# Kernel optimization log

Hardware: AMD Instinct MI355X
Metric: run time of the kernel (lower is better)

Reference implementation:

```python
import jax, jax.numpy as jnp
from jax import lax
import numpy as np

T, N, H, C = 1000, 64, 1024, 256

def setup_inputs() -> dict:
    key = jax.random.key(0)
    k0, k1, k2, k3, k4 = jax.random.split(key, 5)
    s = 0.05
    return {
        "encoder_output": jax.random.normal(k0, (T, N, H), dtype=jnp.float32),
        "W_ih": jax.random.normal(k1, (3 * C, H), dtype=jnp.float32) * s,  # [r|z|n] input weights
        "W_hh": jax.random.normal(k2, (3 * C, C), dtype=jnp.float32) * s,
        "b_ih": jax.random.normal(k3, (3 * C,), dtype=jnp.float32) * s,
        "b_hh": jax.random.normal(k4, (3 * C,), dtype=jnp.float32) * s,
    }

def reference(encoder_output, W_ih, W_hh, b_ih, b_hh):
    # Batched input projection over all timesteps: [T,N,3C]
    xp = jnp.einsum('tnh,gh->tng', encoder_output, W_ih) + b_ih
    c = W_hh.shape[1]

    def step(h, xp_t):
        gh = h @ W_hh.T + b_hh                      # [N,3C]
        xr, xz, xn = jnp.split(xp_t, 3, axis=-1)
        hr, hz, hn = jnp.split(gh, 3, axis=-1)
        r = jax.nn.sigmoid(xr + hr)
        z = jax.nn.sigmoid(xz + hz)
        n = jnp.tanh(xn + r * hn)
        h_new = (1.0 - z) * n + z * h
        return h_new, h_new

    h0 = jnp.zeros((encoder_output.shape[1], c), dtype=encoder_output.dtype)
    _, out = lax.scan(step, h0, xp)                 # out: [T,N,C]
    return jax.nn.log_softmax(out, axis=2)
```

## Files before the change

### kernel.cpp

```cpp
#include <hip/hip_runtime.h>
#include <stdint.h>

#define T_STEPS 1000
#define NB      64
#define HDIM    1024
#define CDIM    256
#define G3      768
#define LOG2E   1.44269504088896340736f

typedef float f32x4  __attribute__((ext_vector_type(4)));
typedef short bf16x8 __attribute__((ext_vector_type(8)));
typedef int   i32x4  __attribute__((ext_vector_type(4)));

__device__ __forceinline__ float bf2f(unsigned short u) {
    union { unsigned int i; float f; } v; v.i = ((unsigned int)u) << 16; return v.f;
}
__device__ __forceinline__ unsigned short f2bf(float f) {
    union { float f; unsigned int i; } v; v.f = f;
    unsigned int r = v.i + 0x7fffu + ((v.i >> 16) & 1u);
    return (unsigned short)(r >> 16);
}

__device__ __forceinline__ int pack4(i32x4 a) {
#if __has_builtin(__builtin_amdgcn_permlane16_swap) && __has_builtin(__builtin_amdgcn_permlane32_swap)
    auto y01 = __builtin_amdgcn_permlane16_swap(a[0], a[1], false, false);
    auto y23 = __builtin_amdgcn_permlane16_swap(a[2], a[3], false, false);
    auto p   = __builtin_amdgcn_permlane32_swap(y01[0], y23[0], false, false);
    return p[0];
#else
    const int lane = threadIdx.x & 63;
    const int l15  = lane & 15;
    const int r1b = __shfl(a[1], l15, 64);
    const int r3b = __shfl(a[3], l15, 64);
    const int x01 = (lane < 16) ? a[0] : r1b;
    const int x23 = (lane < 16) ? a[2] : r3b;
    const int lo  = __shfl(x23, lane & 31, 64);
    return (lane < 32) ? x01 : lo;
#endif
}

__global__ __launch_bounds__(256) void cvt_wih(
    const float* __restrict__ wih, unsigned short* __restrict__ wih_bf)
{
    int idx = blockIdx.x * 256 + threadIdx.x;
    wih_bf[idx] = f2bf(wih[idx]);
}

__global__ __launch_bounds__(64) void quant_whh(
    const float* __restrict__ whh, signed char* __restrict__ wq,
    float* __restrict__ dscale)
{
    const int g    = blockIdx.x;
    const int lane = threadIdx.x;
    const float4 w = *(const float4*)(whh + (size_t)g * CDIM + lane * 4);
    float m = fmaxf(fmaxf(fabsf(w.x), fabsf(w.y)), fmaxf(fabsf(w.z), fabsf(w.w)));
    #pragma unroll
    for (int s = 32; s > 0; s >>= 1) m = fmaxf(m, __shfl_xor(m, s, 64));
    const float inv = (m > 0.f) ? 127.f / m : 0.f;
    char4 q;
    q.x = (signed char)(int)rintf(w.x * inv);
    q.y = (signed char)(int)rintf(w.y * inv);
    q.z = (signed char)(int)rintf(w.z * inv);
    q.w = (signed char)(int)rintf(w.w * inv);
    *(char4*)(wq + (size_t)g * CDIM + lane * 4) = q;
    if (lane == 0) dscale[g] = m / (127.f * 127.f);
}

__global__ __launch_bounds__(256) void xproj_gemm(
    const float* __restrict__ enc,
    const unsigned short* __restrict__ wih,
    const float* __restrict__ bih,
    unsigned short* __restrict__ xp2)
{
    const int gt_base = blockIdx.x * 64;
    const int t       = blockIdx.y;
    const int tid  = threadIdx.x;
    const int w    = tid >> 6;
    const int lane = tid & 63;
    const int q    = lane >> 4, l15 = lane & 15;

    __shared__ unsigned short As[64][72];
    __shared__ unsigned short Bs[64][72];

    const f32x4 zero4 = {0.f, 0.f, 0.f, 0.f};
    f32x4 acc[4] = {zero4, zero4, zero4, zero4};

    const int arow = tid >> 4;
    const int acol = (tid & 15) * 4;
    const int brow = tid >> 3;
    const int bcol = (tid & 7) * 8;

    for (int kt = 0; kt < 16; ++kt) {
        const int k0 = kt * 64;
        __syncthreads();
        #pragma unroll
        for (int i = 0; i < 4; ++i) {
            const int r = arow + i * 16;
            const float4 av = *(const float4*)(enc + (size_t)(t * 64 + r) * HDIM + k0 + acol);
            ushort4 u;
            u.x = f2bf(av.x); u.y = f2bf(av.y); u.z = f2bf(av.z); u.w = f2bf(av.w);
            *(ushort4*)(&As[r][acol]) = u;
        }
        #pragma unroll
        for (int i = 0; i < 2; ++i) {
            const int r = brow + i * 32;
            const uint4 bv = *(const uint4*)(wih + (size_t)(gt_base + r) * HDIM + k0 + bcol);
            *(uint4*)(&Bs[r][bcol]) = bv;
        }
        __syncthreads();
        #pragma unroll
        for (int kk = 0; kk < 2; ++kk) {
            const bf16x8 a = *(const bf16x8*)(&As[16 * w + l15][kk * 32 + q * 8]);
            #pragma unroll
            for (int g = 0; g < 4; ++g) {
                const bf16x8 b = *(const bf16x8*)(&Bs[16 * g + l15][kk * 32 + q * 8]);
                acc[g] = __builtin_amdgcn_mfma_f32_16x16x32_bf16(a, b, acc[g], 0, 0, 0);
            }
        }
    }

    #pragma unroll
    for (int g = 0; g < 4; ++g) {
        const int gg = gt_base + 16 * g + l15;
        const float bias = bih[gg];
        ushort4 u;
        u.x = f2bf(acc[g][0] + bias);
        u.y = f2bf(acc[g][1] + bias);
        u.z = f2bf(acc[g][2] + bias);
        u.w = f2bf(acc[g][3] + bias);
        *(ushort4*)(xp2 + ((size_t)((t * 16 + 4 * w + q) * G3 + gg)) * 4) = u;
    }
}

__global__ void __launch_bounds__(1024)
__attribute__((amdgpu_waves_per_eu(4, 4)))
gru_scan(
    const unsigned short* __restrict__ xp2,
    const signed char* __restrict__ wq,
    const float* __restrict__ dscale,
    const float* __restrict__ bhh,
    float* __restrict__ out)
{
    const int wg   = blockIdx.x;
    const int tid  = threadIdx.x;
    const int wv   = tid >> 6;
    const int lane = tid & 63;
    const int q    = lane >> 4, l15 = lane & 15;
    const int jc   = 16 * wv + l15;

    __shared__ __align__(16) signed char hbuf[2][16][304];

    i32x4 W[3][4];
    float d[3], bh[3];
    #pragma unroll
    for (int s = 0; s < 3; ++s) {
        const int g = 256 * s + jc;
        d[s]  = dscale[g];
        bh[s] = bhh[g];
        #pragma unroll
        for (int kk = 0; kk < 4; ++kk)
            W[s][kk] = *(const i32x4*)(wq + (size_t)g * CDIM + kk * 64 + q * 16);
    }
    #pragma unroll
    for (int s = 0; s < 3; ++s)
        asm volatile("" : "+v"(W[s][0]), "+v"(W[s][1]),
                          "+v"(W[s][2]), "+v"(W[s][3]));

    float h = 0.f;

    for (int i = tid; i < 2 * 16 * 304; i += 1024) ((signed char*)hbuf)[i] = 0;
    __syncthreads();

    unsigned short xc[3];
    {
        const unsigned short* xpt = xp2 + (size_t)wg * (G3 * 4);
        #pragma unroll
        for (int s = 0; s < 3; ++s)
            xc[s] = xpt[(256 * s + jc) * 4 + q];
    }

    int pb = 0;
    for (int t = 0; t < T_STEPS; ++t) {
        const int tn = (t + 1 < T_STEPS) ? t + 1 : t;
        unsigned short xn_[3];
        {
            const unsigned short* xpt = xp2 + ((size_t)tn * 16 + wg) * (G3 * 4);
            #pragma unroll
            for (int s = 0; s < 3; ++s)
                xn_[s] = xpt[(256 * s + jc) * 4 + q];
        }

        i32x4 acc[3];
        #pragma unroll
        for (int s = 0; s < 3; ++s) acc[s] = (i32x4){0, 0, 0, 0};
        #pragma unroll
        for (int kk = 0; kk < 4; ++kk) {
            const i32x4 a = *(const i32x4*)(&hbuf[pb][l15][kk * 64 + q * 16]);
            acc[0] = __builtin_amdgcn_mfma_i32_16x16x64_i8(a, W[0][kk], acc[0], 0, 0, 0);
            acc[1] = __builtin_amdgcn_mfma_i32_16x16x64_i8(a, W[1][kk], acc[1], 0, 0, 0);
            acc[2] = __builtin_amdgcn_mfma_i32_16x16x64_i8(a, W[2][kk], acc[2], 0, 0, 0);
        }

        float P[3];
        #pragma unroll
        for (int s = 0; s < 3; ++s) P[s] = (float)pack4(acc[s]);

        const int pbn = pb ^ 1;
        {
            const float a_r = fmaf(d[0], P[0], bf2f(xc[0]) + bh[0]);
            const float rg  = __builtin_amdgcn_rcpf(
                1.f + __builtin_amdgcn_exp2f(-LOG2E * a_r));
            const float a_z = fmaf(d[1], P[1], bf2f(xc[1]) + bh[1]);
            const float ez  = __builtin_amdgcn_exp2f(-LOG2E * a_z);
            const float zi  = __builtin_amdgcn_rcpf(1.f + ez);
            const float hng = fmaf(d[2], P[2], bh[2]);
            const float na  = fmaf(rg, hng, bf2f(xc[2]));
            const float e2  = __builtin_amdgcn_exp2f(2.f * LOG2E * na);
            const float th  = 1.f - 2.f * __builtin_amdgcn_rcpf(e2 + 1.f);
            const float hv  = zi * fmaf(ez, th, h);
            h = hv;
            hbuf[pbn][q][jc] = (signed char)(int)rintf(hv * 127.f);
            out[((size_t)t * NB + wg * 4 + q) * CDIM + jc] = hv;
        }
        asm volatile("s_waitcnt lgkmcnt(0)\n\ts_barrier" ::: "memory");
        pb = pbn;
        #pragma unroll
        for (int s = 0; s < 3; ++s) xc[s] = xn_[s];
    }
}

__global__ __launch_bounds__(256) void logsoftmax_rows(float* __restrict__ out)
{
    const int tid  = threadIdx.x;
    const int wv   = tid >> 6, lane = tid & 63;
    const int row  = blockIdx.x * 4 + wv;
    float* p = out + (size_t)row * CDIM + lane * 4;
    float4 v = *(const float4*)p;

    float m = fmaxf(fmaxf(v.x, v.y), fmaxf(v.z, v.w));
    #pragma unroll
    for (int s = 32; s > 0; s >>= 1) m = fmaxf(m, __shfl_xor(m, s, 64));

    float sum = __builtin_amdgcn_exp2f((v.x - m) * LOG2E)
              + __builtin_amdgcn_exp2f((v.y - m) * LOG2E)
              + __builtin_amdgcn_exp2f((v.z - m) * LOG2E)
              + __builtin_amdgcn_exp2f((v.w - m) * LOG2E);
    #pragma unroll
    for (int s = 32; s > 0; s >>= 1) sum += __shfl_xor(sum, s, 64);

    const float lse = m + __builtin_amdgcn_logf(sum) * 0.69314718055994531f;
    v.x -= lse; v.y -= lse; v.z -= lse; v.w -= lse;
    *(float4*)p = v;
}

extern "C" void kernel_launch(void* const* d_in, const int* in_sizes, int n_in,
                              void* d_out, int out_size, void* d_ws, size_t ws_size,
                              hipStream_t stream)
{
    const float* enc = (const float*)d_in[0];
    const float* wih = (const float*)d_in[1];
    const float* whh = (const float*)d_in[2];
    const float* bih = (const float*)d_in[3];
    const float* bhh = (const float*)d_in[4];
    float* out = (float*)d_out;

    unsigned short* xp2    = (unsigned short*)d_ws;
    unsigned short* wih_bf = (unsigned short*)((char*)d_ws + 98304000);
    signed char*    whhq   = (signed char*)((char*)d_ws + 99876864);
    float*          dsc    = (float*)((char*)d_ws + 100073472);

    cvt_wih<<<dim3(3072), dim3(256), 0, stream>>>(wih, wih_bf);
    quant_whh<<<dim3(768), dim3(64), 0, stream>>>(whh, whhq, dsc);
    xproj_gemm<<<dim3(12, 1000), dim3(256), 0, stream>>>(enc, wih_bf, bih, xp2);
    gru_scan<<<dim3(16), dim3(1024), 0, stream>>>(xp2, whhq, dsc, bhh, out);
    logsoftmax_rows<<<dim3(16000), dim3(256), 0, stream>>>(out);
}
```

Baseline: 1.470 ms.

## Pre-convert encoder to bf16 for projection GEMM and split scan MFMA chains

```diff
diff --git a/kernel.cpp b/kernel.cpp
--- a/kernel.cpp
+++ b/kernel.cpp
@@ -46,6 +46,19 @@
     wih_bf[idx] = f2bf(wih[idx]);
 }
 
+__global__ __launch_bounds__(256) void cvt_enc(
+    const float* __restrict__ e, unsigned short* __restrict__ eb)
+{
+    const size_t i = ((size_t)blockIdx.x * 256 + threadIdx.x) * 8;
+    const float4 v0 = *(const float4*)(e + i);
+    const float4 v1 = *(const float4*)(e + i + 4);
+    ushort4 u0, u1;
+    u0.x = f2bf(v0.x); u0.y = f2bf(v0.y); u0.z = f2bf(v0.z); u0.w = f2bf(v0.w);
+    u1.x = f2bf(v1.x); u1.y = f2bf(v1.y); u1.z = f2bf(v1.z); u1.w = f2bf(v1.w);
+    *(ushort4*)(eb + i)     = u0;
+    *(ushort4*)(eb + i + 4) = u1;
+}
+
 __global__ __launch_bounds__(64) void quant_whh(
     const float* __restrict__ whh, signed char* __restrict__ wq,
     float* __restrict__ dscale)
@@ -132,6 +145,74 @@
     }
 }
 
+__global__ __launch_bounds__(256) void xproj_gemm_bf(
+    const unsigned short* __restrict__ encb,
+    const unsigned short* __restrict__ wih,
+    const float* __restrict__ bih,
+    unsigned short* __restrict__ xp2)
+{
+    const int gt_base = blockIdx.x * 64;
+    const int t       = blockIdx.y;
+    const int tid  = threadIdx.x;
+    const int w    = tid >> 6;
+    const int lane = tid & 63;
+    const int q    = lane >> 4, l15 = lane & 15;
+
+    __shared__ unsigned short As[64][72];
+    __shared__ unsigned short Bs[64][72];
+
+    const f32x4 zero4 = {0.f, 0.f, 0.f, 0.f};
+    f32x4 acc[4] = {zero4, zero4, zero4, zero4};
+
+    const int srow = tid >> 3;
+    const int scol = (tid & 7) * 8;
+
+    const unsigned short* aptr = encb + (size_t)(t * 64 + srow) * HDIM + scol;
+    const unsigned short* bptr = wih  + (size_t)(gt_base + srow) * HDIM + scol;
+
+    uint4 a0 = *(const uint4*)(aptr);
+    uint4 a1 = *(const uint4*)(aptr + 32 * HDIM);
+    uint4 b0 = *(const uint4*)(bptr);
+    uint4 b1 = *(const uint4*)(bptr + 32 * HDIM);
+
+    for (int kt = 0; kt < 16; ++kt) {
+        __syncthreads();
+        *(uint4*)(&As[srow][scol])      = a0;
+        *(uint4*)(&As[srow + 32][scol]) = a1;
+        *(uint4*)(&Bs[srow][scol])      = b0;
+        *(uint4*)(&Bs[srow + 32][scol]) = b1;
+        __syncthreads();
+        if (kt + 1 < 16) {
+            const int k0n = (kt + 1) * 64;
+            a0 = *(const uint4*)(aptr + k0n);
+            a1 = *(const uint4*)(aptr + 32 * HDIM + k0n);
+            b0 = *(const uint4*)(bptr + k0n);
+            b1 = *(const uint4*)(bptr + 32 * HDIM + k0n);
+        }
+        #pragma unroll
+        for (int kk = 0; kk < 2; ++kk) {
+            const bf16x8 a = *(const bf16x8*)(&As[16 * w + l15][kk * 32 + q * 8]);
+            #pragma unroll
+            for (int g = 0; g < 4; ++g) {
+                const bf16x8 b = *(const bf16x8*)(&Bs[16 * g + l15][kk * 32 + q * 8]);
+                acc[g] = __builtin_amdgcn_mfma_f32_16x16x32_bf16(a, b, acc[g], 0, 0, 0);
+            }
+        }
+    }
+
+    #pragma unroll
+    for (int g = 0; g < 4; ++g) {
+        const int gg = gt_base + 16 * g + l15;
+        const float bias = bih[gg];
+        ushort4 u;
+        u.x = f2bf(acc[g][0] + bias);
+        u.y = f2bf(acc[g][1] + bias);
+        u.z = f2bf(acc[g][2] + bias);
+        u.w = f2bf(acc[g][3] + bias);
+        *(ushort4*)(xp2 + ((size_t)((t * 16 + 4 * w + q) * G3 + gg)) * 4) = u;
+    }
+}
+
 __global__ void __launch_bounds__(1024)
 __attribute__((amdgpu_waves_per_eu(4, 4)))
 gru_scan(
@@ -148,7 +229,7 @@
     const int q    = lane >> 4, l15 = lane & 15;
     const int jc   = 16 * wv + l15;
 
-    __shared__ __align__(16) signed char hbuf[2][16][304];
+    __shared__ __align__(16) signed char hbuf[2][16][320];
 
     i32x4 W[3][4];
     float d[3], bh[3];
@@ -168,7 +249,7 @@
 
     float h = 0.f;
 
-    for (int i = tid; i < 2 * 16 * 304; i += 1024) ((signed char*)hbuf)[i] = 0;
+    for (int i = tid; i < 2 * 16 * 320; i += 1024) ((signed char*)hbuf)[i] = 0;
     __syncthreads();
 
     unsigned short xc[3];
@@ -178,6 +259,10 @@
         for (int s = 0; s < 3; ++s)
             xc[s] = xpt[(256 * s + jc) * 4 + q];
     }
+
+    i32x4 Areg[4];
+    #pragma unroll
+    for (int kk = 0; kk < 4; ++kk) Areg[kk] = (i32x4){0, 0, 0, 0};
 
     int pb = 0;
     for (int t = 0; t < T_STEPS; ++t) {
@@ -190,20 +275,31 @@
                 xn_[s] = xpt[(256 * s + jc) * 4 + q];
         }
 
-        i32x4 acc[3];
-        #pragma unroll
-        for (int s = 0; s < 3; ++s) acc[s] = (i32x4){0, 0, 0, 0};
-        #pragma unroll
-        for (int kk = 0; kk < 4; ++kk) {
-            const i32x4 a = *(const i32x4*)(&hbuf[pb][l15][kk * 64 + q * 16]);
-            acc[0] = __builtin_amdgcn_mfma_i32_16x16x64_i8(a, W[0][kk], acc[0], 0, 0, 0);
-            acc[1] = __builtin_amdgcn_mfma_i32_16x16x64_i8(a, W[1][kk], acc[1], 0, 0, 0);
-            acc[2] = __builtin_amdgcn_mfma_i32_16x16x64_i8(a, W[2][kk], acc[2], 0, 0, 0);
-        }
+        if (l15 < 4) {
+            #pragma unroll
+            for (int kk = 0; kk < 4; ++kk)
+                Areg[kk] = *(const i32x4*)(&hbuf[pb][l15][kk * 64 + q * 16]);
+        }
+
+        i32x4 acA[3], acB[3];
+        #pragma unroll
+        for (int s = 0; s < 3; ++s) { acA[s] = (i32x4){0,0,0,0}; acB[s] = (i32x4){0,0,0,0}; }
+        #pragma unroll
+        for (int s = 0; s < 3; ++s)
+            acA[s] = __builtin_amdgcn_mfma_i32_16x16x64_i8(Areg[0], W[s][0], acA[s], 0, 0, 0);
+        #pragma unroll
+        for (int s = 0; s < 3; ++s)
+            acB[s] = __builtin_amdgcn_mfma_i32_16x16x64_i8(Areg[2], W[s][2], acB[s], 0, 0, 0);
+        #pragma unroll
+        for (int s = 0; s < 3; ++s)
+            acA[s] = __builtin_amdgcn_mfma_i32_16x16x64_i8(Areg[1], W[s][1], acA[s], 0, 0, 0);
+        #pragma unroll
+        for (int s = 0; s < 3; ++s)
+            acB[s] = __builtin_amdgcn_mfma_i32_16x16x64_i8(Areg[3], W[s][3], acB[s], 0, 0, 0);
 
         float P[3];
         #pragma unroll
-        for (int s = 0; s < 3; ++s) P[s] = (float)pack4(acc[s]);
+        for (int s = 0; s < 3; ++s) P[s] = (float)pack4(acA[s] + acB[s]);
 
         const int pbn = pb ^ 1;
         {
@@ -268,10 +364,18 @@
     unsigned short* wih_bf = (unsigned short*)((char*)d_ws + 98304000);
     signed char*    whhq   = (signed char*)((char*)d_ws + 99876864);
     float*          dsc    = (float*)((char*)d_ws + 100073472);
+    unsigned short* enc_bf = (unsigned short*)((char*)d_ws + 100076544);
+
+    const bool big_ws = (ws_size >= 100076544ULL + 131072000ULL);
 
     cvt_wih<<<dim3(3072), dim3(256), 0, stream>>>(wih, wih_bf);
     quant_whh<<<dim3(768), dim3(64), 0, stream>>>(whh, whhq, dsc);
-    xproj_gemm<<<dim3(12, 1000), dim3(256), 0, stream>>>(enc, wih_bf, bih, xp2);
+    if (big_ws) {
+        cvt_enc<<<dim3(32000), dim3(256), 0, stream>>>(enc, enc_bf);
+        xproj_gemm_bf<<<dim3(12, 1000), dim3(256), 0, stream>>>(enc_bf, wih_bf, bih, xp2);
+    } else {
+        xproj_gemm<<<dim3(12, 1000), dim3(256), 0, stream>>>(enc, wih_bf, bih, xp2);
+    }
     gru_scan<<<dim3(16), dim3(1024), 0, stream>>>(xp2, whhq, dsc, bhh, out);
     logsoftmax_rows<<<dim3(16000), dim3(256), 0, stream>>>(out);
 }
```

Result: faster. 1.419 ms (-3.4%).
